# Performance work log

Hardware: AMD Instinct MI355X
Metric: run time of the kernel (lower is better)

The kernel has to match this reference:

```python
import jax, jax.numpy as jnp
import numpy as np

BATCH, IN_F, OUT_F = 8192, 4096, 4096


def setup_inputs() -> dict:
    key = jax.random.key(0)
    kx, kw = jax.random.split(key)
    x = jax.random.normal(kx, (BATCH, IN_F), dtype=jnp.float32)
    # weights binarized to {-1, +1} as in __init__ (uniform(-1,1) then sign)
    W = jnp.where(jax.random.normal(kw, (OUT_F, IN_F)) > 0, 1.0, -1.0).astype(jnp.float32)
    return {"x": x, "W": W}


def reference(x, W):
    # forward: input thresholded to {0,1} (x>0 -> 1, else 0), then x_bin @ W^T, no bias
    x_bin = (x > 0).astype(x.dtype)
    return jnp.matmul(x_bin, W.T)  # [batch, out_features]
```

## Files before the change

kernel.cpp:

```cpp
#include <hip/hip_runtime.h>
#include <stdint.h>

typedef __attribute__((ext_vector_type(4))) int   v4i;
typedef __attribute__((ext_vector_type(8))) int   v8i;
typedef __attribute__((ext_vector_type(4))) float v4f;

#define BATCH 8192
#define KDIM  4096
#define NOUT  4096
#define KB    (KDIM / 2)
#define BK_B  128
#define NT    (KDIM / 256)

__global__ __launch_bounds__(256) void pack_x4(const float* __restrict__ x,
                                               uint32_t* __restrict__ xb) {
    int t = blockIdx.x * 256 + threadIdx.x;
    const float4* p = (const float4*)x + (size_t)t * 2;
    float4 f0 = p[0];
    float4 f1 = p[1];
    uint32_t b = (f0.x > 0.f ? 0x2u        : 0u)
               | (f0.y > 0.f ? 0x20u       : 0u)
               | (f0.z > 0.f ? 0x200u      : 0u)
               | (f0.w > 0.f ? 0x2000u     : 0u)
               | (f1.x > 0.f ? 0x20000u    : 0u)
               | (f1.y > 0.f ? 0x200000u   : 0u)
               | (f1.z > 0.f ? 0x2000000u  : 0u)
               | (f1.w > 0.f ? 0x20000000u : 0u);
    xb[t] = b;
}

__global__ __launch_bounds__(256) void pack_w4(const float* __restrict__ w,
                                               uint32_t* __restrict__ wb) {
    int t = blockIdx.x * 256 + threadIdx.x;
    const float4* p = (const float4*)w + (size_t)t * 2;
    float4 f0 = p[0];
    float4 f1 = p[1];
    uint32_t b = (f0.x > 0.f ? 0x2u        : 0xAu)
               | (f0.y > 0.f ? 0x20u       : 0xA0u)
               | (f0.z > 0.f ? 0x200u      : 0xA00u)
               | (f0.w > 0.f ? 0x2000u     : 0xA000u)
               | (f1.x > 0.f ? 0x20000u    : 0xA0000u)
               | (f1.y > 0.f ? 0x200000u   : 0xA00000u)
               | (f1.z > 0.f ? 0x2000000u  : 0xA000000u)
               | (f1.w > 0.f ? 0x20000000u : 0xA0000000u);
    wb[t] = b;
}

__global__ __launch_bounds__(512, 2) void bin_gemm4(const uint8_t* __restrict__ A,
                                                    const uint8_t* __restrict__ B,
                                                    float* __restrict__ C) {
    __shared__ __align__(16) uint8_t sm[131072];

    const int tid  = threadIdx.x;
    const int w    = tid >> 6;
    const int lane = tid & 63;
    const int q    = lane >> 4;
    const int mp   = lane & 15;

    const int Mbase = blockIdx.y * 256;
    const int Nbase = blockIdx.x * 256;
    const int wm = (w >> 2) * 128;
    const int wn = (w & 3) * 64;

    const int srow = w * 8 + (lane >> 3);
    const int swz  = ((lane & 7) ^ ((lane >> 3) & 7)) * 16;

    const uint8_t* pA = A + (size_t)(Mbase + srow) * KB + swz;
    const uint8_t* pB = B + (size_t)(Nbase + srow) * KB + swz;
    const int ldsw = w * 1024;

    const int rsw = mp & 7;

    v4f acc[8][4] = {};

    #pragma unroll
    for (int L = 0; L < 4; ++L) {
        __builtin_amdgcn_global_load_lds(
            (__attribute__((address_space(1))) void*)(pA + (size_t)(L * 64) * KB),
            (__attribute__((address_space(3))) void*)(sm + L * 8192 + ldsw), 16, 0, 0);
        __builtin_amdgcn_global_load_lds(
            (__attribute__((address_space(1))) void*)(pB + (size_t)(L * 64) * KB),
            (__attribute__((address_space(3))) void*)(sm + 32768 + L * 8192 + ldsw), 16, 0, 0);
    }
    __syncthreads();

    for (int t = 0; t < NT; ++t) {
        if (t + 1 < NT) {
            const int nb  = (t + 1) & 1;
            const int kof = (t + 1) * BK_B;
            #pragma unroll
            for (int L = 0; L < 4; ++L) {
                __builtin_amdgcn_global_load_lds(
                    (__attribute__((address_space(1))) void*)(pA + (size_t)(L * 64) * KB + kof),
                    (__attribute__((address_space(3))) void*)(sm + nb * 65536 + L * 8192 + ldsw),
                    16, 0, 0);
                __builtin_amdgcn_global_load_lds(
                    (__attribute__((address_space(1))) void*)(pB + (size_t)(L * 64) * KB + kof),
                    (__attribute__((address_space(3))) void*)(sm + nb * 65536 + 32768 + L * 8192 + ldsw),
                    16, 0, 0);
            }
        }

        const uint8_t* sA = sm + (t & 1) * 65536;
        const uint8_t* sB = sA + 32768;

        v4i bfr[4][2];
        #pragma unroll
        for (int ni = 0; ni < 4; ++ni)
            #pragma unroll
            for (int ks = 0; ks < 2; ++ks)
                bfr[ni][ks] = *(const v4i*)(sB + (wn + ni * 16 + mp) * 128
                                            + ((ks * 4 + q) ^ rsw) * 16);

        #pragma unroll
        for (int p = 0; p < 4; ++p) {
            v4i afr[2][2];
            #pragma unroll
            for (int i = 0; i < 2; ++i)
                #pragma unroll
                for (int ks = 0; ks < 2; ++ks)
                    afr[i][ks] = *(const v4i*)(sA + (wm + (p * 2 + i) * 16 + mp) * 128
                                               + ((ks * 4 + q) ^ rsw) * 16);
            #pragma unroll
            for (int i = 0; i < 2; ++i)
                #pragma unroll
                for (int ni = 0; ni < 4; ++ni)
                    #pragma unroll
                    for (int ks = 0; ks < 2; ++ks) {
                        v8i a8 = {afr[i][ks][0], afr[i][ks][1], afr[i][ks][2], afr[i][ks][3],
                                  0, 0, 0, 0};
                        v8i b8 = {bfr[ni][ks][0], bfr[ni][ks][1], bfr[ni][ks][2],
                                  bfr[ni][ks][3], 0, 0, 0, 0};
                        acc[p * 2 + i][ni] = __builtin_amdgcn_mfma_scale_f32_16x16x128_f8f6f4(
                            a8, b8, acc[p * 2 + i][ni], 4, 4,
                            0, 0x7F7F7F7F, 0, 0x7F7F7F7F);
                    }
        }

        __syncthreads();
    }

    float* Cp = C + (size_t)(Mbase + wm + q * 4) * NOUT + (Nbase + wn + mp);
    #pragma unroll
    for (int mi = 0; mi < 8; ++mi)
        #pragma unroll
        for (int ni = 0; ni < 4; ++ni)
            #pragma unroll
            for (int r = 0; r < 4; ++r)
                Cp[(size_t)(mi * 16 + r) * NOUT + ni * 16] = acc[mi][ni][r];
}

extern "C" void kernel_launch(void* const* d_in, const int* in_sizes, int n_in,
                              void* d_out, int out_size, void* d_ws, size_t ws_size,
                              hipStream_t stream) {
    const float* x = (const float*)d_in[0];
    const float* W = (const float*)d_in[1];
    float* out = (float*)d_out;

    uint8_t* xb = (uint8_t*)d_ws;
    uint8_t* wb = (uint8_t*)d_ws + (size_t)BATCH * KDIM / 2;

    pack_x4<<<(BATCH * (size_t)KDIM / 8) / 256, 256, 0, stream>>>(x, (uint32_t*)xb);
    pack_w4<<<((size_t)NOUT * KDIM / 8) / 256, 256, 0, stream>>>(W, (uint32_t*)wb);

    dim3 grid(NOUT / 256, BATCH / 256);
    bin_gemm4<<<grid, 512, 0, stream>>>(xb, wb, out);
}
```

Baseline: 322.7 us.

## Restructure GEMM main loop with deeper prefetch, fine-grained barriers and setprio

```diff
diff --git a/kernel.cpp b/kernel.cpp
--- a/kernel.cpp
+++ b/kernel.cpp
@@ -82,38 +82,34 @@
             (__attribute__((address_space(1))) void*)(pB + (size_t)(L * 64) * KB),
             (__attribute__((address_space(3))) void*)(sm + 32768 + L * 8192 + ldsw), 16, 0, 0);
     }
-    __syncthreads();
-
-    for (int t = 0; t < NT; ++t) {
-        if (t + 1 < NT) {
-            const int nb  = (t + 1) & 1;
-            const int kof = (t + 1) * BK_B;
-            #pragma unroll
-            for (int L = 0; L < 4; ++L) {
-                __builtin_amdgcn_global_load_lds(
-                    (__attribute__((address_space(1))) void*)(pA + (size_t)(L * 64) * KB + kof),
-                    (__attribute__((address_space(3))) void*)(sm + nb * 65536 + L * 8192 + ldsw),
-                    16, 0, 0);
-                __builtin_amdgcn_global_load_lds(
-                    (__attribute__((address_space(1))) void*)(pB + (size_t)(L * 64) * KB + kof),
-                    (__attribute__((address_space(3))) void*)(sm + nb * 65536 + 32768 + L * 8192 + ldsw),
-                    16, 0, 0);
-            }
-        }
+    #pragma unroll
+    for (int L = 0; L < 4; ++L) {
+        __builtin_amdgcn_global_load_lds(
+            (__attribute__((address_space(1))) void*)(pA + (size_t)(L * 64) * KB + BK_B),
+            (__attribute__((address_space(3))) void*)(sm + 65536 + L * 8192 + ldsw), 16, 0, 0);
+        __builtin_amdgcn_global_load_lds(
+            (__attribute__((address_space(1))) void*)(pB + (size_t)(L * 64) * KB + BK_B),
+            (__attribute__((address_space(3))) void*)(sm + 65536 + 32768 + L * 8192 + ldsw), 16, 0, 0);
+    }
+
+    for (int t = 0; t < NT - 1; ++t) {
+        asm volatile("s_waitcnt vmcnt(8)" ::: "memory");
+        __builtin_amdgcn_s_barrier();
 
         const uint8_t* sA = sm + (t & 1) * 65536;
         const uint8_t* sB = sA + 32768;
 
         v4i bfr[4][2];
         #pragma unroll
-        for (int ni = 0; ni < 4; ++ni)
-            #pragma unroll
-            for (int ks = 0; ks < 2; ++ks)
-                bfr[ni][ks] = *(const v4i*)(sB + (wn + ni * 16 + mp) * 128
-                                            + ((ks * 4 + q) ^ rsw) * 16);
-
-        #pragma unroll
         for (int p = 0; p < 4; ++p) {
+            if (p == 0) {
+                #pragma unroll
+                for (int ni = 0; ni < 4; ++ni)
+                    #pragma unroll
+                    for (int ks = 0; ks < 2; ++ks)
+                        bfr[ni][ks] = *(const v4i*)(sB + (wn + ni * 16 + mp) * 128
+                                                    + ((ks * 4 + q) ^ rsw) * 16);
+            }
             v4i afr[2][2];
             #pragma unroll
             for (int i = 0; i < 2; ++i)
@@ -121,6 +117,10 @@
                 for (int ks = 0; ks < 2; ++ks)
                     afr[i][ks] = *(const v4i*)(sA + (wm + (p * 2 + i) * 16 + mp) * 128
                                                + ((ks * 4 + q) ^ rsw) * 16);
+
+            __builtin_amdgcn_s_barrier();
+            asm volatile("s_waitcnt lgkmcnt(0)" ::: "memory");
+            __builtin_amdgcn_s_setprio(1);
             #pragma unroll
             for (int i = 0; i < 2; ++i)
                 #pragma unroll
@@ -135,9 +135,70 @@
                             a8, b8, acc[p * 2 + i][ni], 4, 4,
                             0, 0x7F7F7F7F, 0, 0x7F7F7F7F);
                     }
+            __builtin_amdgcn_s_setprio(0);
+            __builtin_amdgcn_s_barrier();
         }
 
-        __syncthreads();
+        if (t < NT - 2) {
+            const int kof = (t + 2) * BK_B;
+            uint8_t* db = (uint8_t*)sm + (t & 1) * 65536;
+            #pragma unroll
+            for (int L = 0; L < 4; ++L) {
+                __builtin_amdgcn_global_load_lds(
+                    (__attribute__((address_space(1))) void*)(pA + (size_t)(L * 64) * KB + kof),
+                    (__attribute__((address_space(3))) void*)(db + L * 8192 + ldsw), 16, 0, 0);
+                __builtin_amdgcn_global_load_lds(
+                    (__attribute__((address_space(1))) void*)(pB + (size_t)(L * 64) * KB + kof),
+                    (__attribute__((address_space(3))) void*)(db + 32768 + L * 8192 + ldsw), 16, 0, 0);
+            }
+        }
+    }
+
+    asm volatile("s_waitcnt vmcnt(0)" ::: "memory");
+    __builtin_amdgcn_s_barrier();
+    {
+        const uint8_t* sA = sm + ((NT - 1) & 1) * 65536;
+        const uint8_t* sB = sA + 32768;
+
+        v4i bfr[4][2];
+        #pragma unroll
+        for (int p = 0; p < 4; ++p) {
+            if (p == 0) {
+                #pragma unroll
+                for (int ni = 0; ni < 4; ++ni)
+                    #pragma unroll
+                    for (int ks = 0; ks < 2; ++ks)
+                        bfr[ni][ks] = *(const v4i*)(sB + (wn + ni * 16 + mp) * 128
+                                                    + ((ks * 4 + q) ^ rsw) * 16);
+            }
+            v4i afr[2][2];
+            #pragma unroll
+            for (int i = 0; i < 2; ++i)
+                #pragma unroll
+                for (int ks = 0; ks < 2; ++ks)
+                    afr[i][ks] = *(const v4i*)(sA + (wm + (p * 2 + i) * 16 + mp) * 128
+                                               + ((ks * 4 + q) ^ rsw) * 16);
+
+            __builtin_amdgcn_s_barrier();
+            asm volatile("s_waitcnt lgkmcnt(0)" ::: "memory");
+            __builtin_amdgcn_s_setprio(1);
+            #pragma unroll
+            for (int i = 0; i < 2; ++i)
+                #pragma unroll
+                for (int ni = 0; ni < 4; ++ni)
+                    #pragma unroll
+                    for (int ks = 0; ks < 2; ++ks) {
+                        v8i a8 = {afr[i][ks][0], afr[i][ks][1], afr[i][ks][2], afr[i][ks][3],
+                                  0, 0, 0, 0};
+                        v8i b8 = {bfr[ni][ks][0], bfr[ni][ks][1], bfr[ni][ks][2],
+                                  bfr[ni][ks][3], 0, 0, 0, 0};
+                        acc[p * 2 + i][ni] = __builtin_amdgcn_mfma_scale_f32_16x16x128_f8f6f4(
+                            a8, b8, acc[p * 2 + i][ni], 4, 4,
+                            0, 0x7F7F7F7F, 0, 0x7F7F7F7F);
+                    }
+            __builtin_amdgcn_s_setprio(0);
+            __builtin_amdgcn_s_barrier();
+        }
     }
 
     float* Cp = C + (size_t)(Mbase + wm + q * 4) * NOUT + (Nbase + wn + mp);
```

Result: slower. 333.2 us (+3.3%).

## Switch FP4 GEMM inner loop to 32x32x64 scaled MFMA tiles

Applied to the files above, without the earlier changes.

```diff
diff --git a/kernel.cpp b/kernel.cpp
--- a/kernel.cpp
+++ b/kernel.cpp
@@ -1,9 +1,9 @@
 #include <hip/hip_runtime.h>
 #include <stdint.h>
 
-typedef __attribute__((ext_vector_type(4))) int   v4i;
-typedef __attribute__((ext_vector_type(8))) int   v8i;
-typedef __attribute__((ext_vector_type(4))) float v4f;
+typedef __attribute__((ext_vector_type(4)))  int   v4i;
+typedef __attribute__((ext_vector_type(8)))  int   v8i;
+typedef __attribute__((ext_vector_type(16))) float v16f;
 
 #define BATCH 8192
 #define KDIM  4096
@@ -54,8 +54,9 @@
     const int tid  = threadIdx.x;
     const int w    = tid >> 6;
     const int lane = tid & 63;
-    const int q    = lane >> 4;
-    const int mp   = lane & 15;
+    const int l31  = lane & 31;
+    const int kc   = lane >> 5;
+    const int rsw  = lane & 7;
 
     const int Mbase = blockIdx.y * 256;
     const int Nbase = blockIdx.x * 256;
@@ -69,9 +70,7 @@
     const uint8_t* pB = B + (size_t)(Nbase + srow) * KB + swz;
     const int ldsw = w * 1024;
 
-    const int rsw = mp & 7;
-
-    v4f acc[8][4] = {};
+    v16f acc[4][2] = {};
 
     #pragma unroll
     for (int L = 0; L < 4; ++L) {
@@ -86,17 +85,17 @@
 
     for (int t = 0; t < NT; ++t) {
         if (t + 1 < NT) {
-            const int nb  = (t + 1) & 1;
-            const int kof = (t + 1) * BK_B;
+            const int nbuf = (t + 1) & 1;
+            const int kof  = (t + 1) * BK_B;
             #pragma unroll
             for (int L = 0; L < 4; ++L) {
                 __builtin_amdgcn_global_load_lds(
                     (__attribute__((address_space(1))) void*)(pA + (size_t)(L * 64) * KB + kof),
-                    (__attribute__((address_space(3))) void*)(sm + nb * 65536 + L * 8192 + ldsw),
+                    (__attribute__((address_space(3))) void*)(sm + nbuf * 65536 + L * 8192 + ldsw),
                     16, 0, 0);
                 __builtin_amdgcn_global_load_lds(
                     (__attribute__((address_space(1))) void*)(pB + (size_t)(L * 64) * KB + kof),
-                    (__attribute__((address_space(3))) void*)(sm + nb * 65536 + 32768 + L * 8192 + ldsw),
+                    (__attribute__((address_space(3))) void*)(sm + nbuf * 65536 + 32768 + L * 8192 + ldsw),
                     16, 0, 0);
             }
         }
@@ -104,50 +103,40 @@
         const uint8_t* sA = sm + (t & 1) * 65536;
         const uint8_t* sB = sA + 32768;
 
-        v4i bfr[4][2];
         #pragma unroll
-        for (int ni = 0; ni < 4; ++ni)
+        for (int ks = 0; ks < 4; ++ks) {
+            v4i bf[2];
             #pragma unroll
-            for (int ks = 0; ks < 2; ++ks)
-                bfr[ni][ks] = *(const v4i*)(sB + (wn + ni * 16 + mp) * 128
-                                            + ((ks * 4 + q) ^ rsw) * 16);
-
-        #pragma unroll
-        for (int p = 0; p < 4; ++p) {
-            v4i afr[2][2];
+            for (int nb = 0; nb < 2; ++nb)
+                bf[nb] = *(const v4i*)(sB + (wn + nb * 32 + l31) * 128
+                                       + ((ks * 2 + kc) ^ rsw) * 16);
             #pragma unroll
-            for (int i = 0; i < 2; ++i)
+            for (int mb = 0; mb < 4; ++mb) {
+                v4i af = *(const v4i*)(sA + (wm + mb * 32 + l31) * 128
+                                       + ((ks * 2 + kc) ^ rsw) * 16);
+                v8i a8 = {af[0], af[1], af[2], af[3], 0, 0, 0, 0};
                 #pragma unroll
-                for (int ks = 0; ks < 2; ++ks)
-                    afr[i][ks] = *(const v4i*)(sA + (wm + (p * 2 + i) * 16 + mp) * 128
-                                               + ((ks * 4 + q) ^ rsw) * 16);
-            #pragma unroll
-            for (int i = 0; i < 2; ++i)
-                #pragma unroll
-                for (int ni = 0; ni < 4; ++ni)
-                    #pragma unroll
-                    for (int ks = 0; ks < 2; ++ks) {
-                        v8i a8 = {afr[i][ks][0], afr[i][ks][1], afr[i][ks][2], afr[i][ks][3],
-                                  0, 0, 0, 0};
-                        v8i b8 = {bfr[ni][ks][0], bfr[ni][ks][1], bfr[ni][ks][2],
-                                  bfr[ni][ks][3], 0, 0, 0, 0};
-                        acc[p * 2 + i][ni] = __builtin_amdgcn_mfma_scale_f32_16x16x128_f8f6f4(
-                            a8, b8, acc[p * 2 + i][ni], 4, 4,
-                            0, 0x7F7F7F7F, 0, 0x7F7F7F7F);
-                    }
+                for (int nb = 0; nb < 2; ++nb) {
+                    v8i b8 = {bf[nb][0], bf[nb][1], bf[nb][2], bf[nb][3], 0, 0, 0, 0};
+                    acc[mb][nb] = __builtin_amdgcn_mfma_scale_f32_32x32x64_f8f6f4(
+                        a8, b8, acc[mb][nb], 4, 4,
+                        0, 0x7F7F7F7F, 0, 0x7F7F7F7F);
+                }
+            }
         }
 
         __syncthreads();
     }
 
-    float* Cp = C + (size_t)(Mbase + wm + q * 4) * NOUT + (Nbase + wn + mp);
+    float* Cp = C + (size_t)(Mbase + wm + 4 * kc) * NOUT + (Nbase + wn + l31);
     #pragma unroll
-    for (int mi = 0; mi < 8; ++mi)
+    for (int mb = 0; mb < 4; ++mb)
         #pragma unroll
-        for (int ni = 0; ni < 4; ++ni)
+        for (int nb = 0; nb < 2; ++nb)
             #pragma unroll
-            for (int r = 0; r < 4; ++r)
-                Cp[(size_t)(mi * 16 + r) * NOUT + ni * 16] = acc[mi][ni][r];
+            for (int r = 0; r < 16; ++r)
+                Cp[(size_t)(mb * 32 + (r & 3) + 8 * (r >> 2)) * NOUT + nb * 32]
+                    = acc[mb][nb][r];
 }
 
 extern "C" void kernel_launch(void* const* d_in, const int* in_sizes, int n_in,
```

New measurement: 324.5 us. Within noise of the previous version (+0.6%).
